# Kernel tuning notes

Hardware: AMD Instinct MI355X
Metric: run time of the kernel (lower is better)

The kernel has to match this reference:

```python
import jax, jax.numpy as jnp
import numpy as np

HIDDEN = 1024
NUM_HEADS = 16
HEAD_DIM = HIDDEN // NUM_HEADS  # 64
B, S = 2, 2048


def setup_inputs() -> dict:
    key = jax.random.key(0)
    ks = jax.random.split(key, 10)
    sd = 1.0 / np.sqrt(HIDDEN)
    x = jax.random.normal(ks[0], (B, S, HIDDEN), dtype=jnp.float32)
    # per-head projections stacked over head axis: [H, hidden, head_dim]
    Wq = jax.random.normal(ks[1], (NUM_HEADS, HIDDEN, HEAD_DIM), dtype=jnp.float32) * sd
    Wk = jax.random.normal(ks[2], (NUM_HEADS, HIDDEN, HEAD_DIM), dtype=jnp.float32) * sd
    Wv = jax.random.normal(ks[3], (NUM_HEADS, HIDDEN, HEAD_DIM), dtype=jnp.float32) * sd
    bq = jax.random.normal(ks[4], (NUM_HEADS, HEAD_DIM), dtype=jnp.float32) * sd
    bk = jax.random.normal(ks[5], (NUM_HEADS, HEAD_DIM), dtype=jnp.float32) * sd
    bv = jax.random.normal(ks[6], (NUM_HEADS, HEAD_DIM), dtype=jnp.float32) * sd
    # output projection: [all_head_size, hidden]
    Wo = jax.random.normal(ks[7], (HIDDEN, HIDDEN), dtype=jnp.float32) * sd
    bo = jax.random.normal(ks[8], (HIDDEN,), dtype=jnp.float32) * sd
    return {"x": x, "Wq": Wq, "bq": bq, "Wk": Wk, "bk": bk,
            "Wv": Wv, "bv": bv, "Wo": Wo, "bo": bo}


def reference(x, Wq, bq, Wk, bk, Wv, bv, Wo, bo):
    # Fused-across-heads equivalent of the per-head Python loop.
    # q,k,v: [B, H, S, Dh]
    q = jnp.einsum('bsd,hde->bhse', x, Wq) + bq[None, :, None, :]
    k = jnp.einsum('bsd,hde->bhse', x, Wk) + bk[None, :, None, :]
    v = jnp.einsum('bsd,hde->bhse', x, Wv) + bv[None, :, None, :]
    scale = 1.0 / jnp.sqrt(jnp.asarray(HEAD_DIM, dtype=x.dtype))
    scores = jnp.einsum('bhse,bhte->bhst', q, k) * scale  # [B,H,S,S]
    probs = jax.nn.softmax(scores, axis=-1)               # dropout=0 (eval)
    ctx = jnp.einsum('bhst,bhte->bhse', probs, v)         # [B,H,S,Dh]
    # concat heads on last dim (head order matches torch.cat over heads)
    ctx = jnp.transpose(ctx, (0, 2, 1, 3)).reshape(x.shape[0], x.shape[1], -1)
    out = ctx @ Wo + bo                                   # output projection
    return out
```

## Files before the change

kernel.cpp:

```cpp
#include <hip/hip_runtime.h>
#include <cstdint>

typedef unsigned short u16;
typedef __attribute__((ext_vector_type(8))) short short8;
typedef __attribute__((ext_vector_type(4))) short short4v;
typedef __attribute__((ext_vector_type(4))) float f32x4;
typedef __attribute__((ext_vector_type(4))) unsigned short u16x4;

__device__ __forceinline__ u16 f2bf(float x) {
    unsigned int u = __float_as_uint(x);
    u += 0x7fffu + ((u >> 16) & 1u);
    return (u16)(u >> 16);
}

__device__ __forceinline__ float fexp2(float x) {
#if __has_builtin(__builtin_amdgcn_exp2f)
    return __builtin_amdgcn_exp2f(x);
#else
    return exp2f(x);
#endif
}

__device__ __forceinline__ unsigned pack_bf16(float a, float b) {
    unsigned ua = __float_as_uint(a) + 0x8000u;
    unsigned ub = __float_as_uint(b) + 0x8000u;
    return __builtin_amdgcn_perm(ub, ua, 0x07060302u);
}

#if __has_builtin(__builtin_amdgcn_mfma_f32_16x16x16bf16_1k)
__device__ __forceinline__ f32x4 mfma16(short4v a, short4v b, f32x4 c) {
    return __builtin_amdgcn_mfma_f32_16x16x16bf16_1k(a, b, c, 0, 0, 0);
}
#else
__device__ __forceinline__ f32x4 mfma16(short4v a, short4v b, f32x4 c) {
    short8 a8 = {a[0], a[1], a[2], a[3], 0, 0, 0, 0};
    short8 b8 = {b[0], b[1], b[2], b[3], 0, 0, 0, 0};
    return __builtin_amdgcn_mfma_f32_16x16x32_bf16(a8, b8, c, 0, 0, 0);
}
#endif

__device__ __forceinline__ void gload_lds16(const u16* g, u16* l) {
    __builtin_amdgcn_global_load_lds(
        (const __attribute__((address_space(1))) void*)(g),
        (__attribute__((address_space(3))) void*)(l),
        16, 0, 0);
}

__global__ __launch_bounds__(256) void prep_kernel(
    const float* __restrict__ x,
    const float* __restrict__ Wq, const float* __restrict__ Wk,
    const float* __restrict__ Wv, const float* __restrict__ Wo,
    u16* __restrict__ xb, u16* __restrict__ wqkv, u16* __restrict__ wot)
{
    __shared__ u16 tile[64][65];
    const int z = blockIdx.z;
    const int tc = threadIdx.x & 63, tr = threadIdx.x >> 6;

    if (z == 1) {
        const int blk = blockIdx.y * 16 + blockIdx.x;
        const int base = (blk * 256 + threadIdx.x) * 4;
        #pragma unroll
        for (int i = 0; i < 16; ++i) {
            const int idx = base + i * 262144;
            float4 v = *(const float4*)(x + idx);
            u16x4 o;
            o.x = f2bf(v.x); o.y = f2bf(v.y); o.z = f2bf(v.z); o.w = f2bf(v.w);
            *(u16x4*)(xb + idx) = o;
        }
        return;
    }

    const float* src;
    u16* dst;
    int C, R, rb, cb;
    if (z == 0) {
        src = Wo; dst = wot; C = 1024; R = 1024;
        rb = blockIdx.x * 64; cb = blockIdx.y * 64;
    } else {
        const float* W = (z == 2) ? Wq : (z == 3) ? Wk : Wv;
        const int head = blockIdx.y;
        src = W + head * 65536;
        dst = wqkv + (size_t)(z - 2) * 1048576 + head * 65536;
        C = 64; R = 1024;
        rb = blockIdx.x * 64; cb = 0;
    }
    #pragma unroll
    for (int i = 0; i < 64; i += 4)
        tile[tr + i][tc] = f2bf(src[(size_t)(rb + tr + i) * C + (cb + tc)]);
    __syncthreads();
    #pragma unroll
    for (int i = 0; i < 64; i += 4)
        dst[(size_t)(cb + tr + i) * R + (rb + tc)] = tile[tc][tr + i];
}

__global__ __launch_bounds__(256, 3) void gemm_qkv_kernel(
    const u16* __restrict__ X, const u16* __restrict__ W,
    const float* __restrict__ bq, const float* __restrict__ bk,
    const float* __restrict__ bv,
    u16* __restrict__ qo, u16* __restrict__ ko, u16* __restrict__ vto)
{
    __shared__ __align__(16) u16 As[128 * 32];
    __shared__ __align__(16) u16 Bs[128 * 32];
    const int tid = threadIdx.x;
    const int lane = tid & 63;
    const int wv = tid >> 6;
    const int wm = wv & 1, wn = wv >> 1;
    const int m0 = blockIdx.y * 128;
    const int n0 = blockIdx.x * 128;
    const int c = lane & 15, qd = lane >> 4;

    f32x4 acc[4][4];
    #pragma unroll
    for (int a = 0; a < 4; ++a)
        #pragma unroll
        for (int b2 = 0; b2 < 4; ++b2) acc[a][b2] = f32x4{0.f, 0.f, 0.f, 0.f};

    const u16* Xb = X + (size_t)m0 * 1024;
    const u16* Wb = W + (size_t)n0 * 1024;

    for (int kt = 0; kt < 1024; kt += 32) {
        #pragma unroll
        for (int i = 0; i < 2; ++i) {
            int slot = i * 256 + tid;
            int row = slot >> 2, part = slot & 3;
            gload_lds16(Xb + (size_t)row * 1024 + kt + part * 8, &As[slot * 8]);
            gload_lds16(Wb + (size_t)row * 1024 + kt + part * 8, &Bs[slot * 8]);
        }
        __syncthreads();
        short8 af[4], bf[4];
        #pragma unroll
        for (int mt = 0; mt < 4; ++mt)
            af[mt] = *(const short8*)&As[(wm * 64 + mt * 16 + c) * 32 + qd * 8];
        #pragma unroll
        for (int nt = 0; nt < 4; ++nt)
            bf[nt] = *(const short8*)&Bs[(wn * 64 + nt * 16 + c) * 32 + qd * 8];
        #pragma unroll
        for (int mt = 0; mt < 4; ++mt)
            #pragma unroll
            for (int nt = 0; nt < 4; ++nt)
                acc[mt][nt] = __builtin_amdgcn_mfma_f32_16x16x32_bf16(af[mt], bf[nt], acc[mt][nt], 0, 0, 0);
        __syncthreads();
    }

    #pragma unroll
    for (int mt = 0; mt < 4; ++mt) {
        const int mbase = m0 + wm * 64 + mt * 16 + qd * 4;
        const int b = mbase >> 11;
        #pragma unroll
        for (int nt = 0; nt < 4; ++nt) {
            const int n = n0 + wn * 64 + nt * 16 + c;
            const int mat = n >> 10;
            const int idx = n & 1023;
            const int h = idx >> 6, e = idx & 63;
            const float bias = (mat == 0 ? bq : (mat == 1 ? bk : bv))[idx];
            if (mat == 2) {
                const int s = mbase & 2047;
                u16x4 pv;
                pv.x = f2bf(acc[mt][nt][0] + bias);
                pv.y = f2bf(acc[mt][nt][1] + bias);
                pv.z = f2bf(acc[mt][nt][2] + bias);
                pv.w = f2bf(acc[mt][nt][3] + bias);
                *(u16x4*)(vto + ((((size_t)(b * 16 + h) * 128 + (s >> 4)) * 64 + e) * 16
                                 + (s & 15))) = pv;
            } else {
                const float scale = (mat == 0) ? 0.18033688011112042f : 1.0f;
                u16* dst = (mat == 0) ? qo : ko;
                #pragma unroll
                for (int r = 0; r < 4; ++r) {
                    const int s = (mbase + r) & 2047;
                    dst[((size_t)((b * 16 + h) * 2048 + s)) * 64 + e] =
                        f2bf((acc[mt][nt][r] + bias) * scale);
                }
            }
        }
    }
}

__global__ __launch_bounds__(256, 3) void flash_kernel(
    const u16* __restrict__ Q,
    const u16* __restrict__ K,
    const u16* __restrict__ V2,
    u16* __restrict__ ctx)
{
    __shared__ __align__(16) char pool[49152];
    u16* stage = (u16*)pool;
    float (*Os)[64][66] = (float (*)[64][66])pool;
    float (*Ls)[64] = (float (*)[64])(pool + 33792);

    const int tid = threadIdx.x, lane = tid & 63, w = tid >> 6;
    const int c = lane & 15, qd = lane >> 4;
    const int bid = blockIdx.x;
    const int r5 = bid & 31;
    const int bh = (r5 & 7) * 4 + (r5 >> 3);
    const int q0 = (bid >> 5) * 64;
    const int b = bh >> 4, h = bh & 15;
    const u16* Qh = Q + (size_t)bh * 2048 * 64;
    const u16* Kh = K + (size_t)bh * 2048 * 64;
    const u16* Vh = V2 + (size_t)bh * 128 * 1024;

    u16* Kst = stage + w * 6144;
    u16* Vst = Kst + 3072;

    const int krow8 = lane >> 3;
    const int kgc = (lane & 7) ^ (krow8 & 7);

    short8 qf[4][2];
    #pragma unroll
    for (int qb = 0; qb < 4; ++qb)
        #pragma unroll
        for (int kb = 0; kb < 2; ++kb)
            qf[qb][kb] = *(const short8*)&Qh[(size_t)(q0 + qb * 16 + c) * 64 + kb * 32 + qd * 8];

    f32x4 o[4][4];
    f32x4 ol[4];
    #pragma unroll
    for (int mt = 0; mt < 4; ++mt)
        #pragma unroll
        for (int qb = 0; qb < 4; ++qb) o[mt][qb] = f32x4{0.f, 0.f, 0.f, 0.f};
    #pragma unroll
    for (int qb = 0; qb < 4; ++qb) ol[qb] = f32x4{0.f, 0.f, 0.f, 0.f};
    const short4v ones = {(short)0x3F80, (short)0x3F80, (short)0x3F80, (short)0x3F80};

    #pragma unroll
    for (int pit = 0; pit < 2; ++pit) {
        const int t0 = w * 512 + pit * 16;
        #pragma unroll
        for (int j = 0; j < 2; ++j) {
            const int row = j * 8 + krow8;
            gload_lds16(Kh + (size_t)(t0 + row) * 64 + kgc * 8,
                        Kst + pit * 1024 + j * 512 + lane * 8);
            gload_lds16(Vh + (size_t)(t0 >> 4) * 1024 + (j * 64 + lane) * 8,
                        Vst + pit * 1024 + j * 512 + lane * 8);
        }
    }

    int cur = 0;
    for (int it = 0; it < 32; ++it) {
        u16* Kb = Kst + cur * 1024;
        u16* Vb = Vst + cur * 1024;

        __builtin_amdgcn_s_waitcnt(0xF74);
        __builtin_amdgcn_sched_barrier(0);

        short8 kf[2];
        #pragma unroll
        for (int kb = 0; kb < 2; ++kb)
            kf[kb] = *(const short8*)&Kb[c * 64 + ((4 * kb + qd) ^ (c & 7)) * 8];
        short4v vf[4];
        #pragma unroll
        for (int mt = 0; mt < 4; ++mt)
            vf[mt] = *(const short4v*)&Vb[(mt * 16 + c) * 16 + qd * 4];

        __builtin_amdgcn_sched_barrier(0);

        {
            const int itn = (it + 2) & 31;
            const int t0n = w * 512 + itn * 16;
            const int nslot = (cur >= 1) ? cur - 1 : 2;
            u16* Kn = Kst + nslot * 1024;
            u16* Vn = Vst + nslot * 1024;
            #pragma unroll
            for (int j = 0; j < 2; ++j) {
                const int row = j * 8 + krow8;
                gload_lds16(Kh + (size_t)(t0n + row) * 64 + kgc * 8,
                            Kn + j * 512 + lane * 8);
                gload_lds16(Vh + (size_t)(t0n >> 4) * 1024 + (j * 64 + lane) * 8,
                            Vn + j * 512 + lane * 8);
            }
        }

        f32x4 sc[4];
        #pragma unroll
        for (int qb = 0; qb < 4; ++qb) {
            sc[qb] = f32x4{0.f, 0.f, 0.f, 0.f};
            sc[qb] = __builtin_amdgcn_mfma_f32_16x16x32_bf16(kf[0], qf[qb][0], sc[qb], 0, 0, 0);
            sc[qb] = __builtin_amdgcn_mfma_f32_16x16x32_bf16(kf[1], qf[qb][1], sc[qb], 0, 0, 0);
        }

        short4v pb[4];
        #pragma unroll
        for (int qb = 0; qb < 4; ++qb) {
            float p0 = fexp2(sc[qb][0]);
            float p1 = fexp2(sc[qb][1]);
            float p2 = fexp2(sc[qb][2]);
            float p3 = fexp2(sc[qb][3]);
            unsigned d0 = pack_bf16(p0, p1);
            unsigned d1 = pack_bf16(p2, p3);
            union { unsigned u[2]; short4v s; } pu;
            pu.u[0] = d0; pu.u[1] = d1;
            pb[qb] = pu.s;
        }

        #pragma unroll
        for (int qb = 0; qb < 4; ++qb) {
            #pragma unroll
            for (int mt = 0; mt < 4; ++mt)
                o[mt][qb] = mfma16(vf[mt], pb[qb], o[mt][qb]);
            ol[qb] = mfma16(ones, pb[qb], ol[qb]);
        }

        cur = (cur == 2) ? 0 : cur + 1;
    }

    __builtin_amdgcn_s_waitcnt(0xF70);
    __syncthreads();
    if (qd == 0) {
        #pragma unroll
        for (int qb = 0; qb < 4; ++qb) Ls[w][qb * 16 + c] = ol[qb][0];
    }

    if (w >= 2) {
        float (*S)[66] = Os[w - 2];
        #pragma unroll
        for (int mt = 0; mt < 4; ++mt)
            #pragma unroll
            for (int qb = 0; qb < 4; ++qb)
                #pragma unroll
                for (int r = 0; r < 4; ++r)
                    S[mt * 16 + qd * 4 + r][qb * 16 + c] = o[mt][qb][r];
    }
    __syncthreads();
    if (w < 2) {
        float (*S)[66] = Os[w];
        #pragma unroll
        for (int mt = 0; mt < 4; ++mt)
            #pragma unroll
            for (int qb = 0; qb < 4; ++qb)
                #pragma unroll
                for (int r = 0; r < 4; ++r)
                    o[mt][qb][r] += S[mt * 16 + qd * 4 + r][qb * 16 + c];
    }
    __syncthreads();
    if (w == 1) {
        float (*S)[66] = Os[0];
        #pragma unroll
        for (int mt = 0; mt < 4; ++mt)
            #pragma unroll
            for (int qb = 0; qb < 4; ++qb)
                #pragma unroll
                for (int r = 0; r < 4; ++r)
                    S[mt * 16 + qd * 4 + r][qb * 16 + c] = o[mt][qb][r];
    }
    __syncthreads();
    if (w == 0) {
        float (*S)[66] = Os[0];
        float inv[4];
        #pragma unroll
        for (int qb = 0; qb < 4; ++qb) {
            int q = qb * 16 + c;
            float l = (Ls[0][q] + Ls[1][q]) + (Ls[2][q] + Ls[3][q]);
            inv[qb] = __builtin_amdgcn_rcpf(l);
        }
        #pragma unroll
        for (int mt = 0; mt < 4; ++mt)
            #pragma unroll
            for (int qb = 0; qb < 4; ++qb) {
                u16x4 ov;
                #pragma unroll
                for (int r = 0; r < 4; ++r) {
                    float v = (o[mt][qb][r] + S[mt * 16 + qd * 4 + r][qb * 16 + c]) * inv[qb];
                    ((u16*)&ov)[r] = f2bf(v);
                }
                *(u16x4*)&ctx[((size_t)(b * 2048 + q0 + qb * 16 + c)) * 1024
                              + h * 64 + mt * 16 + qd * 4] = ov;
            }
    }
}

__global__ __launch_bounds__(256, 4) void gemm_out_kernel(
    const u16* __restrict__ A, const u16* __restrict__ Wt,
    const float* __restrict__ bo, float* __restrict__ out)
{
    __shared__ __align__(16) u16 As[64 * 32];
    __shared__ __align__(16) u16 Bs[128 * 32];
    const int tid = threadIdx.x;
    const int lane = tid & 63;
    const int wv = tid >> 6;
    const int wm = wv & 1, wn = wv >> 1;
    const int m0 = blockIdx.x * 64;
    const int n0 = blockIdx.y * 128;
    const int c = lane & 15, qd = lane >> 4;

    f32x4 acc[2][4];
    #pragma unroll
    for (int a = 0; a < 2; ++a)
        #pragma unroll
        for (int b2 = 0; b2 < 4; ++b2) acc[a][b2] = f32x4{0.f, 0.f, 0.f, 0.f};

    const u16* Ab = A + (size_t)m0 * 1024;
    const u16* Wb = Wt + (size_t)n0 * 1024;

    for (int kt = 0; kt < 1024; kt += 32) {
        {
            int row = tid >> 2, part = tid & 3;
            gload_lds16(Ab + (size_t)row * 1024 + kt + part * 8, &As[tid * 8]);
        }
        #pragma unroll
        for (int i = 0; i < 2; ++i) {
            int slot = i * 256 + tid;
            int row = slot >> 2, part = slot & 3;
            gload_lds16(Wb + (size_t)row * 1024 + kt + part * 8, &Bs[slot * 8]);
        }
        __syncthreads();
        short8 af[2], bf[4];
        #pragma unroll
        for (int mt = 0; mt < 2; ++mt)
            af[mt] = *(const short8*)&As[(wm * 32 + mt * 16 + c) * 32 + qd * 8];
        #pragma unroll
        for (int nt = 0; nt < 4; ++nt)
            bf[nt] = *(const short8*)&Bs[(wn * 64 + nt * 16 + c) * 32 + qd * 8];
        #pragma unroll
        for (int mt = 0; mt < 2; ++mt)
            #pragma unroll
            for (int nt = 0; nt < 4; ++nt)
                acc[mt][nt] = __builtin_amdgcn_mfma_f32_16x16x32_bf16(af[mt], bf[nt], acc[mt][nt], 0, 0, 0);
        __syncthreads();
    }

    #pragma unroll
    for (int mt = 0; mt < 2; ++mt) {
        const int mbase = m0 + wm * 32 + mt * 16 + qd * 4;
        #pragma unroll
        for (int nt = 0; nt < 4; ++nt) {
            const int n = n0 + wn * 64 + nt * 16 + c;
            const float bias = bo[n];
            #pragma unroll
            for (int r = 0; r < 4; ++r)
                out[(size_t)(mbase + r) * 1024 + n] = acc[mt][nt][r] + bias;
        }
    }
}

extern "C" void kernel_launch(void* const* d_in, const int* in_sizes, int n_in,
                              void* d_out, int out_size, void* d_ws, size_t ws_size,
                              hipStream_t stream) {
    const float* x  = (const float*)d_in[0];
    const float* Wq = (const float*)d_in[1];
    const float* bq = (const float*)d_in[2];
    const float* Wk = (const float*)d_in[3];
    const float* bk = (const float*)d_in[4];
    const float* Wv = (const float*)d_in[5];
    const float* bv = (const float*)d_in[6];
    const float* Wo = (const float*)d_in[7];
    const float* bo = (const float*)d_in[8];
    float* out = (float*)d_out;

    u16* ws    = (u16*)d_ws;
    u16* xb    = ws;
    u16* wqkv  = xb + 4096 * 1024;
    u16* wot   = wqkv + 3072 * 1024;
    u16* qws   = wot + 1024 * 1024;
    u16* kws   = qws + 4194304;
    u16* v2ws  = kws + 4194304;
    u16* ctxws = v2ws + 4194304;

    prep_kernel<<<dim3(16, 16, 5), 256, 0, stream>>>(x, Wq, Wk, Wv, Wo, xb, wqkv, wot);
    gemm_qkv_kernel<<<dim3(24, 32), 256, 0, stream>>>(xb, wqkv, bq, bk, bv, qws, kws, v2ws);
    flash_kernel<<<1024, 256, 0, stream>>>(qws, kws, v2ws, ctxws);
    gemm_out_kernel<<<dim3(64, 8), 256, 0, stream>>>(ctxws, wot, bo, out);
}
```

Baseline: 190.7 us.

## Pre-swizzle K into MFMA fragment layout and load K/V directly to registers

The QKV GEMM epilogue now writes K in a fragment-ordered layout, so the flash kernel can load K and V operands straight from global memory into registers. This replaces the previous LDS staging pipeline that used global_load_lds and waitcnt. The PV product now uses the 16x16x32 MFMA on two key tiles at once, with P round-tripped through a small per-wave LDS buffer to reach the B-operand layout. LDS use drops, which could raise occupancy, but global load latency is now hidden only by register prefetching one iteration ahead.

```diff
diff --git a/kernel.cpp b/kernel.cpp
--- a/kernel.cpp
+++ b/kernel.cpp
@@ -3,7 +3,6 @@
 
 typedef unsigned short u16;
 typedef __attribute__((ext_vector_type(8))) short short8;
-typedef __attribute__((ext_vector_type(4))) short short4v;
 typedef __attribute__((ext_vector_type(4))) float f32x4;
 typedef __attribute__((ext_vector_type(4))) unsigned short u16x4;
 
@@ -26,18 +25,6 @@
     unsigned ub = __float_as_uint(b) + 0x8000u;
     return __builtin_amdgcn_perm(ub, ua, 0x07060302u);
 }
-
-#if __has_builtin(__builtin_amdgcn_mfma_f32_16x16x16bf16_1k)
-__device__ __forceinline__ f32x4 mfma16(short4v a, short4v b, f32x4 c) {
-    return __builtin_amdgcn_mfma_f32_16x16x16bf16_1k(a, b, c, 0, 0, 0);
-}
-#else
-__device__ __forceinline__ f32x4 mfma16(short4v a, short4v b, f32x4 c) {
-    short8 a8 = {a[0], a[1], a[2], a[3], 0, 0, 0, 0};
-    short8 b8 = {b[0], b[1], b[2], b[3], 0, 0, 0, 0};
-    return __builtin_amdgcn_mfma_f32_16x16x32_bf16(a8, b8, c, 0, 0, 0);
-}
-#endif
 
 __device__ __forceinline__ void gload_lds16(const u16* g, u16* l) {
     __builtin_amdgcn_global_load_lds(
@@ -146,6 +133,7 @@
     for (int mt = 0; mt < 4; ++mt) {
         const int mbase = m0 + wm * 64 + mt * 16 + qd * 4;
         const int b = mbase >> 11;
+        const int s0 = mbase & 2047;
         #pragma unroll
         for (int nt = 0; nt < 4; ++nt) {
             const int n = n0 + wn * 64 + nt * 16 + c;
@@ -154,21 +142,28 @@
             const int h = idx >> 6, e = idx & 63;
             const float bias = (mat == 0 ? bq : (mat == 1 ? bk : bv))[idx];
             if (mat == 2) {
-                const int s = mbase & 2047;
                 u16x4 pv;
                 pv.x = f2bf(acc[mt][nt][0] + bias);
                 pv.y = f2bf(acc[mt][nt][1] + bias);
                 pv.z = f2bf(acc[mt][nt][2] + bias);
                 pv.w = f2bf(acc[mt][nt][3] + bias);
-                *(u16x4*)(vto + ((((size_t)(b * 16 + h) * 128 + (s >> 4)) * 64 + e) * 16
-                                 + (s & 15))) = pv;
+                *(u16x4*)(vto + ((((size_t)(b * 16 + h) * 128 + (s0 >> 4)) * 64 + e) * 16
+                                 + (s0 & 15))) = pv;
+            } else if (mat == 1) {
+                const size_t kfb = ((size_t)(b * 16 + h)) * 131072
+                                 + (size_t)(s0 >> 4) * 1024
+                                 + (size_t)(e >> 5) * 512
+                                 + (size_t)((((e >> 3) & 3) * 16 + (s0 & 15))) * 8
+                                 + (e & 7);
+                #pragma unroll
+                for (int r = 0; r < 4; ++r)
+                    ko[kfb + r * 8] = f2bf(acc[mt][nt][r] + bias);
             } else {
-                const float scale = (mat == 0) ? 0.18033688011112042f : 1.0f;
-                u16* dst = (mat == 0) ? qo : ko;
+                const float scale = 0.18033688011112042f;
                 #pragma unroll
                 for (int r = 0; r < 4; ++r) {
-                    const int s = (mbase + r) & 2047;
-                    dst[((size_t)((b * 16 + h) * 2048 + s)) * 64 + e] =
+                    const int s = s0 + r;
+                    qo[((size_t)((b * 16 + h) * 2048 + s)) * 64 + e] =
                         f2bf((acc[mt][nt][r] + bias) * scale);
                 }
             }
@@ -178,12 +173,12 @@
 
 __global__ __launch_bounds__(256, 3) void flash_kernel(
     const u16* __restrict__ Q,
-    const u16* __restrict__ K,
+    const u16* __restrict__ Kf,
     const u16* __restrict__ V2,
     u16* __restrict__ ctx)
 {
-    __shared__ __align__(16) char pool[49152];
-    u16* stage = (u16*)pool;
+    __shared__ __align__(16) char pool[34816];
+    u16* Pall = (u16*)pool;
     float (*Os)[64][66] = (float (*)[64][66])pool;
     float (*Ls)[64] = (float (*)[64])(pool + 33792);
 
@@ -194,15 +189,10 @@
     const int bh = (r5 & 7) * 4 + (r5 >> 3);
     const int q0 = (bid >> 5) * 64;
     const int b = bh >> 4, h = bh & 15;
-    const u16* Qh = Q + (size_t)bh * 2048 * 64;
-    const u16* Kh = K + (size_t)bh * 2048 * 64;
-    const u16* Vh = V2 + (size_t)bh * 128 * 1024;
-
-    u16* Kst = stage + w * 6144;
-    u16* Vst = Kst + 3072;
-
-    const int krow8 = lane >> 3;
-    const int kgc = (lane & 7) ^ (krow8 & 7);
+    const u16* Qh = Q + (size_t)bh * 131072;
+    const u16* Kh = Kf + (size_t)bh * 131072;
+    const u16* Vh = V2 + (size_t)bh * 131072;
+    u16* Pw = Pall + w * 2560;
 
     short8 qf[4][2];
     #pragma unroll
@@ -219,90 +209,68 @@
         for (int qb = 0; qb < 4; ++qb) o[mt][qb] = f32x4{0.f, 0.f, 0.f, 0.f};
     #pragma unroll
     for (int qb = 0; qb < 4; ++qb) ol[qb] = f32x4{0.f, 0.f, 0.f, 0.f};
-    const short4v ones = {(short)0x3F80, (short)0x3F80, (short)0x3F80, (short)0x3F80};
-
-    #pragma unroll
-    for (int pit = 0; pit < 2; ++pit) {
-        const int t0 = w * 512 + pit * 16;
-        #pragma unroll
-        for (int j = 0; j < 2; ++j) {
-            const int row = j * 8 + krow8;
-            gload_lds16(Kh + (size_t)(t0 + row) * 64 + kgc * 8,
-                        Kst + pit * 1024 + j * 512 + lane * 8);
-            gload_lds16(Vh + (size_t)(t0 >> 4) * 1024 + (j * 64 + lane) * 8,
-                        Vst + pit * 1024 + j * 512 + lane * 8);
-        }
-    }
-
-    int cur = 0;
-    for (int it = 0; it < 32; ++it) {
-        u16* Kb = Kst + cur * 1024;
-        u16* Vb = Vst + cur * 1024;
-
-        __builtin_amdgcn_s_waitcnt(0xF74);
-        __builtin_amdgcn_sched_barrier(0);
-
-        short8 kf[2];
+    const short8 ones8 = {(short)0x3F80, (short)0x3F80, (short)0x3F80, (short)0x3F80,
+                          (short)0x3F80, (short)0x3F80, (short)0x3F80, (short)0x3F80};
+
+    const size_t koff = (size_t)lane * 8;
+    const size_t voff = (size_t)(c + ((qd >> 1) << 6)) * 16 + (qd & 1) * 8;
+
+    const int gbase = w * 32;
+    short8 kf[2][2], vf[4];
+    #pragma unroll
+    for (int T = 0; T < 2; ++T)
         #pragma unroll
         for (int kb = 0; kb < 2; ++kb)
-            kf[kb] = *(const short8*)&Kb[c * 64 + ((4 * kb + qd) ^ (c & 7)) * 8];
-        short4v vf[4];
-        #pragma unroll
-        for (int mt = 0; mt < 4; ++mt)
-            vf[mt] = *(const short4v*)&Vb[(mt * 16 + c) * 16 + qd * 4];
-
-        __builtin_amdgcn_sched_barrier(0);
-
-        {
-            const int itn = (it + 2) & 31;
-            const int t0n = w * 512 + itn * 16;
-            const int nslot = (cur >= 1) ? cur - 1 : 2;
-            u16* Kn = Kst + nslot * 1024;
-            u16* Vn = Vst + nslot * 1024;
-            #pragma unroll
-            for (int j = 0; j < 2; ++j) {
-                const int row = j * 8 + krow8;
-                gload_lds16(Kh + (size_t)(t0n + row) * 64 + kgc * 8,
-                            Kn + j * 512 + lane * 8);
-                gload_lds16(Vh + (size_t)(t0n >> 4) * 1024 + (j * 64 + lane) * 8,
-                            Vn + j * 512 + lane * 8);
+            kf[T][kb] = *(const short8*)&Kh[(size_t)(gbase + T) * 1024 + kb * 512 + koff];
+    #pragma unroll
+    for (int mt = 0; mt < 4; ++mt)
+        vf[mt] = *(const short8*)&Vh[(size_t)gbase * 1024 + (size_t)mt * 256 + voff];
+
+    for (int it = 0; it < 16; ++it) {
+        const int gn = gbase + ((it + 1) & 15) * 2;
+
+        #pragma unroll
+        for (int T = 0; T < 2; ++T) {
+            f32x4 sc[4];
+            #pragma unroll
+            for (int qb = 0; qb < 4; ++qb) {
+                sc[qb] = f32x4{0.f, 0.f, 0.f, 0.f};
+                sc[qb] = __builtin_amdgcn_mfma_f32_16x16x32_bf16(kf[T][0], qf[qb][0], sc[qb], 0, 0, 0);
+                sc[qb] = __builtin_amdgcn_mfma_f32_16x16x32_bf16(kf[T][1], qf[qb][1], sc[qb], 0, 0, 0);
             }
-        }
-
-        f32x4 sc[4];
+            #pragma unroll
+            for (int qb = 0; qb < 4; ++qb) {
+                float p0 = fexp2(sc[qb][0]);
+                float p1 = fexp2(sc[qb][1]);
+                float p2 = fexp2(sc[qb][2]);
+                float p3 = fexp2(sc[qb][3]);
+                union { unsigned u[2]; u16x4 v; } pu;
+                pu.u[0] = pack_bf16(p0, p1);
+                pu.u[1] = pack_bf16(p2, p3);
+                *(u16x4*)&Pw[(qb * 16 + c) * 40 + T * 16 + qd * 4] = pu.v;
+            }
+        }
+
+        #pragma unroll
+        for (int T = 0; T < 2; ++T)
+            #pragma unroll
+            for (int kb = 0; kb < 2; ++kb)
+                kf[T][kb] = *(const short8*)&Kh[(size_t)(gn + T) * 1024 + kb * 512 + koff];
+
         #pragma unroll
         for (int qb = 0; qb < 4; ++qb) {
-            sc[qb] = f32x4{0.f, 0.f, 0.f, 0.f};
-            sc[qb] = __builtin_amdgcn_mfma_f32_16x16x32_bf16(kf[0], qf[qb][0], sc[qb], 0, 0, 0);
-            sc[qb] = __builtin_amdgcn_mfma_f32_16x16x32_bf16(kf[1], qf[qb][1], sc[qb], 0, 0, 0);
-        }
-
-        short4v pb[4];
-        #pragma unroll
-        for (int qb = 0; qb < 4; ++qb) {
-            float p0 = fexp2(sc[qb][0]);
-            float p1 = fexp2(sc[qb][1]);
-            float p2 = fexp2(sc[qb][2]);
-            float p3 = fexp2(sc[qb][3]);
-            unsigned d0 = pack_bf16(p0, p1);
-            unsigned d1 = pack_bf16(p2, p3);
-            union { unsigned u[2]; short4v s; } pu;
-            pu.u[0] = d0; pu.u[1] = d1;
-            pb[qb] = pu.s;
-        }
-
-        #pragma unroll
-        for (int qb = 0; qb < 4; ++qb) {
+            short8 pB = *(const short8*)&Pw[(qb * 16 + c) * 40 + qd * 8];
             #pragma unroll
             for (int mt = 0; mt < 4; ++mt)
-                o[mt][qb] = mfma16(vf[mt], pb[qb], o[mt][qb]);
-            ol[qb] = mfma16(ones, pb[qb], ol[qb]);
-        }
-
-        cur = (cur == 2) ? 0 : cur + 1;
-    }
-
-    __builtin_amdgcn_s_waitcnt(0xF70);
+                o[mt][qb] = __builtin_amdgcn_mfma_f32_16x16x32_bf16(vf[mt], pB, o[mt][qb], 0, 0, 0);
+            ol[qb] = __builtin_amdgcn_mfma_f32_16x16x32_bf16(ones8, pB, ol[qb], 0, 0, 0);
+        }
+
+        #pragma unroll
+        for (int mt = 0; mt < 4; ++mt)
+            vf[mt] = *(const short8*)&Vh[(size_t)gn * 1024 + (size_t)mt * 256 + voff];
+    }
+
     __syncthreads();
     if (qd == 0) {
         #pragma unroll
@@ -450,12 +418,12 @@
     u16* wqkv  = xb + 4096 * 1024;
     u16* wot   = wqkv + 3072 * 1024;
     u16* qws   = wot + 1024 * 1024;
-    u16* kws   = qws + 4194304;
-    u16* v2ws  = kws + 4194304;
+    u16* kfws  = qws + 4194304;
+    u16* v2ws  = kfws + 4194304;
     u16* ctxws = v2ws + 4194304;
 
     prep_kernel<<<dim3(16, 16, 5), 256, 0, stream>>>(x, Wq, Wk, Wv, Wo, xb, wqkv, wot);
-    gemm_qkv_kernel<<<dim3(24, 32), 256, 0, stream>>>(xb, wqkv, bq, bk, bv, qws, kws, v2ws);
-    flash_kernel<<<1024, 256, 0, stream>>>(qws, kws, v2ws, ctxws);
+    gemm_qkv_kernel<<<dim3(24, 32), 256, 0, stream>>>(xb, wqkv, bq, bk, bv, qws, kfws, v2ws);
+    flash_kernel<<<1024, 256, 0, stream>>>(qws, kfws, v2ws, ctxws);
     gemm_out_kernel<<<dim3(64, 8), 256, 0, stream>>>(ctxws, wot, bo, out);
 }
```

New measurement: 192.6 us. No clear change (+1.0%).
